# Optimization experiments

Hardware: AMD Instinct MI355X
Metric: run time of the kernel (lower is better)

Reference implementation:

```python
import jax, jax.numpy as jnp
import numpy as np

B, F, D = 16384, 40, 32

def setup_inputs() -> dict:
    key = jax.random.key(0)
    k1, k2, k3, k4 = jax.random.split(key, 4)
    g = jax.random.uniform(k1, (B, F, F), dtype=jnp.float32)
    h = jax.random.normal(k2, (B, F, D), dtype=jnp.float32)
    # Xavier-normal init for per-field [D,D] weights: std = sqrt(2/(D+D))
    std = float(np.sqrt(2.0 / (D + D)))
    W_in = jax.random.normal(k3, (F, D, D), dtype=jnp.float32) * std
    W_out = jax.random.normal(k4, (F, D, D), dtype=jnp.float32) * std
    bias_p = jnp.zeros((D,), dtype=jnp.float32)
    return {"g": g, "h": h, "W_in": W_in, "W_out": W_out, "bias_p": bias_p}

def reference(g, h, W_in, W_out, bias_p):
    # per-field transform: [F,D,D] x [B,F,D] -> [B,F,D]
    h_out = jnp.einsum('fde,bfe->bfd', W_out, h)
    # graph aggregation over fields: [B,F,F] x [B,F,D] -> [B,F,D]
    aggr = jnp.einsum('bfg,bgd->bfd', g, h_out)
    # per-field transform + bias
    a = jnp.einsum('fde,bfe->bfd', W_in, aggr) + bias_p
    return a
```

## Files before the change

### kernel.cpp

```cpp
#include <hip/hip_runtime.h>


#define B_TOT 16384
#define FF    40
#define DD    32

template<bool ADD_BIAS, bool IN_PLACE>
__global__ __launch_bounds__(256)
void field_transform(const float* __restrict__ W,
                     const float* __restrict__ src,
                     const float* __restrict__ bias,
                     float* __restrict__ dst)
{
    const int f = blockIdx.y;
    const int b = blockIdx.x * 256 + threadIdx.x;
    const float* wf = W + (size_t)f * (DD * DD);
    const float* srow = (IN_PLACE ? (const float*)dst : src)
                        + ((size_t)b * FF + f) * DD;

    float4 hr[8];
    #pragma unroll
    for (int j = 0; j < 8; ++j) hr[j] = ((const float4*)srow)[j];

    float acc[DD];
    #pragma unroll
    for (int d = 0; d < DD; ++d) {
        const float4* wrow = (const float4*)(wf + d * DD);
        float s = 0.f;
        #pragma unroll
        for (int j = 0; j < 8; ++j) {
            float4 w = wrow[j];
            s += w.x * hr[j].x + w.y * hr[j].y + w.z * hr[j].z + w.w * hr[j].w;
        }
        if (ADD_BIAS) s += bias[d];
        acc[d] = s;
    }

    float* drow = dst + ((size_t)b * FF + f) * DD;
    #pragma unroll
    for (int j = 0; j < 8; ++j)
        ((float4*)drow)[j] = make_float4(acc[4*j+0], acc[4*j+1],
                                         acc[4*j+2], acc[4*j+3]);
}

__global__ __launch_bounds__(256)
void graph_aggr(const float* __restrict__ g,
                float* __restrict__ io)
{
    __shared__ __attribute__((aligned(16))) float s_ho[4 * FF * DD];
    const int t  = threadIdx.x;
    const int b0 = blockIdx.x * 4;

    const float4* src = (const float4*)(io + (size_t)b0 * (FF * DD));
    #pragma unroll
    for (int k = 0; k < 5; ++k)
        ((float4*)s_ho)[t + k * 256] = src[t + k * 256];
    __syncthreads();

    const int w  = t >> 6;
    const int l  = t & 63;
    const int dg = l >> 3;
    const int fg = l & 7;

    const float* gb   = g + (size_t)(b0 + w) * (FF * FF);
    const float* shob = s_ho + w * (FF * DD);

    float acc[5][4];
    #pragma unroll
    for (int i = 0; i < 5; ++i)
        #pragma unroll
        for (int j = 0; j < 4; ++j) acc[i][j] = 0.f;

    for (int gc = 0; gc < 10; ++gc) {
        const int gg = gc << 2;
        float4 gv[5];
        #pragma unroll
        for (int i = 0; i < 5; ++i)
            gv[i] = *(const float4*)(gb + (fg + (i << 3)) * FF + gg);
        float4 hv0 = *(const float4*)(shob + (gg + 0) * DD + dg * 4);
        float4 hv1 = *(const float4*)(shob + (gg + 1) * DD + dg * 4);
        float4 hv2 = *(const float4*)(shob + (gg + 2) * DD + dg * 4);
        float4 hv3 = *(const float4*)(shob + (gg + 3) * DD + dg * 4);
        #pragma unroll
        for (int i = 0; i < 5; ++i) {
            acc[i][0] += gv[i].x * hv0.x + gv[i].y * hv1.x + gv[i].z * hv2.x + gv[i].w * hv3.x;
            acc[i][1] += gv[i].x * hv0.y + gv[i].y * hv1.y + gv[i].z * hv2.y + gv[i].w * hv3.y;
            acc[i][2] += gv[i].x * hv0.z + gv[i].y * hv1.z + gv[i].z * hv2.z + gv[i].w * hv3.z;
            acc[i][3] += gv[i].x * hv0.w + gv[i].y * hv1.w + gv[i].z * hv2.w + gv[i].w * hv3.w;
        }
    }

    #pragma unroll
    for (int i = 0; i < 5; ++i) {
        const int f = fg + (i << 3);
        *(float4*)(io + ((size_t)(b0 + w) * FF + f) * DD + dg * 4) =
            make_float4(acc[i][0], acc[i][1], acc[i][2], acc[i][3]);
    }
}

extern "C" void kernel_launch(void* const* d_in, const int* in_sizes, int n_in,
                              void* d_out, int out_size, void* d_ws, size_t ws_size,
                              hipStream_t stream) {
    const float* g    = (const float*)d_in[0];
    const float* h    = (const float*)d_in[1];
    const float* Win  = (const float*)d_in[2];
    const float* Wout = (const float*)d_in[3];
    const float* bias = (const float*)d_in[4];
    float* out = (float*)d_out;

    dim3 block(256);
    dim3 gridFT(B_TOT / 256, FF);
    dim3 gridAG(B_TOT / 4);

    field_transform<false, false><<<gridFT, block, 0, stream>>>(Wout, h, bias, out);
    graph_aggr<<<gridAG, block, 0, stream>>>(g, out);
    field_transform<true, true><<<gridFT, block, 0, stream>>>(Win, nullptr, bias, out);
}
```

Measured before the change: 400.3 us.

## Fuse field transforms and graph aggregation into a single kernel

Measured after the change: 526.0 us. 1.31x slower.

```diff
diff --git a/kernel.cpp b/kernel.cpp
--- a/kernel.cpp
+++ b/kernel.cpp
@@ -4,97 +4,127 @@
 #define B_TOT 16384
 #define FF    40
 #define DD    32
+#define NB    8
+#define WF    10
 
-template<bool ADD_BIAS, bool IN_PLACE>
 __global__ __launch_bounds__(256)
-void field_transform(const float* __restrict__ W,
-                     const float* __restrict__ src,
-                     const float* __restrict__ bias,
-                     float* __restrict__ dst)
+void graph_layer_fused(const float* __restrict__ g,
+                       const float* __restrict__ h,
+                       const float* __restrict__ Win,
+                       const float* __restrict__ Wout,
+                       const float* __restrict__ bias,
+                       float* __restrict__ out)
 {
-    const int f = blockIdx.y;
-    const int b = blockIdx.x * 256 + threadIdx.x;
-    const float* wf = W + (size_t)f * (DD * DD);
-    const float* srow = (IN_PLACE ? (const float*)dst : src)
-                        + ((size_t)b * FF + f) * DD;
+    __shared__ __attribute__((aligned(16))) float s_ho[NB * FF * DD];
 
-    float4 hr[8];
-    #pragma unroll
-    for (int j = 0; j < 8; ++j) hr[j] = ((const float4*)srow)[j];
+    const int t     = threadIdx.x;
+    const int w     = t >> 6;
+    const int l     = t & 63;
+    const int b0    = blockIdx.x * NB;
+    const int fbase = w * WF;
 
-    float acc[DD];
-    #pragma unroll
-    for (int d = 0; d < DD; ++d) {
-        const float4* wrow = (const float4*)(wf + d * DD);
-        float s = 0.f;
+    {
+        const int d    = l & 31;
+        const int half = l >> 5;
+        #pragma unroll 1
+        for (int fi = 0; fi < WF; ++fi) {
+            const int f = fbase + fi;
+            const float4* wrow = (const float4*)(Wout + (size_t)(f * DD + d) * DD);
+            float4 wr[8];
+            #pragma unroll
+            for (int j = 0; j < 8; ++j) wr[j] = wrow[j];
+            #pragma unroll
+            for (int bp = 0; bp < NB / 2; ++bp) {
+                const int bl = 2 * bp + half;
+                const float4* hrow =
+                    (const float4*)(h + ((size_t)(b0 + bl) * FF + f) * DD);
+                float acc = 0.f;
+                #pragma unroll
+                for (int j = 0; j < 8; ++j) {
+                    float4 hv = hrow[j];
+                    acc += wr[j].x * hv.x + wr[j].y * hv.y
+                         + wr[j].z * hv.z + wr[j].w * hv.w;
+                }
+                s_ho[(bl * FF + f) * DD + d] = acc;
+            }
+        }
+    }
+    __syncthreads();
+
+    {
+        const int bl = l >> 3;
+        const int dq = l & 7;
+        const float* grow = g + (size_t)(b0 + bl) * (FF * FF) + (size_t)fbase * FF;
+        const float* shob = s_ho + bl * (FF * DD) + dq * 4;
+
+        float4 acc[WF];
         #pragma unroll
-        for (int j = 0; j < 8; ++j) {
-            float4 w = wrow[j];
-            s += w.x * hr[j].x + w.y * hr[j].y + w.z * hr[j].z + w.w * hr[j].w;
+        for (int fi = 0; fi < WF; ++fi) acc[fi] = make_float4(0.f, 0.f, 0.f, 0.f);
+
+        float4 gv[WF];
+        #pragma unroll
+        for (int fi = 0; fi < WF; ++fi)
+            gv[fi] = *(const float4*)(grow + fi * FF);
+
+        #pragma unroll 1
+        for (int gc = 0; gc < 10; ++gc) {
+            float4 hv[4];
+            #pragma unroll
+            for (int i = 0; i < 4; ++i)
+                hv[i] = *(const float4*)(shob + (4 * gc + i) * DD);
+
+            float4 gn[WF];
+            if (gc < 9) {
+                #pragma unroll
+                for (int fi = 0; fi < WF; ++fi)
+                    gn[fi] = *(const float4*)(grow + fi * FF + 4 * gc + 4);
+            }
+
+            #pragma unroll
+            for (int fi = 0; fi < WF; ++fi) {
+                float4 gf = gv[fi];
+                acc[fi].x += gf.x*hv[0].x + gf.y*hv[1].x + gf.z*hv[2].x + gf.w*hv[3].x;
+                acc[fi].y += gf.x*hv[0].y + gf.y*hv[1].y + gf.z*hv[2].y + gf.w*hv[3].y;
+                acc[fi].z += gf.x*hv[0].z + gf.y*hv[1].z + gf.z*hv[2].z + gf.w*hv[3].z;
+                acc[fi].w += gf.x*hv[0].w + gf.y*hv[1].w + gf.z*hv[2].w + gf.w*hv[3].w;
+            }
+            #pragma unroll
+            for (int fi = 0; fi < WF; ++fi) gv[fi] = gn[fi];
         }
-        if (ADD_BIAS) s += bias[d];
-        acc[d] = s;
+
+        #pragma unroll
+        for (int fi = 0; fi < WF; ++fi)
+            *(float4*)(out + ((size_t)(b0 + bl) * FF + fbase + fi) * DD + dq * 4)
+                = acc[fi];
     }
 
-    float* drow = dst + ((size_t)b * FF + f) * DD;
-    #pragma unroll
-    for (int j = 0; j < 8; ++j)
-        ((float4*)drow)[j] = make_float4(acc[4*j+0], acc[4*j+1],
-                                         acc[4*j+2], acc[4*j+3]);
-}
+    asm volatile("s_waitcnt vmcnt(0)" ::: "memory");
 
-__global__ __launch_bounds__(256)
-void graph_aggr(const float* __restrict__ g,
-                float* __restrict__ io)
-{
-    __shared__ __attribute__((aligned(16))) float s_ho[4 * FF * DD];
-    const int t  = threadIdx.x;
-    const int b0 = blockIdx.x * 4;
-
-    const float4* src = (const float4*)(io + (size_t)b0 * (FF * DD));
-    #pragma unroll
-    for (int k = 0; k < 5; ++k)
-        ((float4*)s_ho)[t + k * 256] = src[t + k * 256];
-    __syncthreads();
-
-    const int w  = t >> 6;
-    const int l  = t & 63;
-    const int dg = l >> 3;
-    const int fg = l & 7;
-
-    const float* gb   = g + (size_t)(b0 + w) * (FF * FF);
-    const float* shob = s_ho + w * (FF * DD);
-
-    float acc[5][4];
-    #pragma unroll
-    for (int i = 0; i < 5; ++i)
-        #pragma unroll
-        for (int j = 0; j < 4; ++j) acc[i][j] = 0.f;
-
-    for (int gc = 0; gc < 10; ++gc) {
-        const int gg = gc << 2;
-        float4 gv[5];
-        #pragma unroll
-        for (int i = 0; i < 5; ++i)
-            gv[i] = *(const float4*)(gb + (fg + (i << 3)) * FF + gg);
-        float4 hv0 = *(const float4*)(shob + (gg + 0) * DD + dg * 4);
-        float4 hv1 = *(const float4*)(shob + (gg + 1) * DD + dg * 4);
-        float4 hv2 = *(const float4*)(shob + (gg + 2) * DD + dg * 4);
-        float4 hv3 = *(const float4*)(shob + (gg + 3) * DD + dg * 4);
-        #pragma unroll
-        for (int i = 0; i < 5; ++i) {
-            acc[i][0] += gv[i].x * hv0.x + gv[i].y * hv1.x + gv[i].z * hv2.x + gv[i].w * hv3.x;
-            acc[i][1] += gv[i].x * hv0.y + gv[i].y * hv1.y + gv[i].z * hv2.y + gv[i].w * hv3.y;
-            acc[i][2] += gv[i].x * hv0.z + gv[i].y * hv1.z + gv[i].z * hv2.z + gv[i].w * hv3.z;
-            acc[i][3] += gv[i].x * hv0.w + gv[i].y * hv1.w + gv[i].z * hv2.w + gv[i].w * hv3.w;
+    {
+        const int d    = l & 31;
+        const int half = l >> 5;
+        const float bv = bias[d];
+        #pragma unroll 1
+        for (int fi = 0; fi < WF; ++fi) {
+            const int f = fbase + fi;
+            const float4* wrow = (const float4*)(Win + (size_t)(f * DD + d) * DD);
+            float4 wr[8];
+            #pragma unroll
+            for (int j = 0; j < 8; ++j) wr[j] = wrow[j];
+            #pragma unroll
+            for (int bp = 0; bp < NB / 2; ++bp) {
+                const int bl = 2 * bp + half;
+                float* arow = out + ((size_t)(b0 + bl) * FF + f) * DD;
+                float acc = bv;
+                #pragma unroll
+                for (int j = 0; j < 8; ++j) {
+                    float4 av = ((const float4*)arow)[j];
+                    acc += wr[j].x * av.x + wr[j].y * av.y
+                         + wr[j].z * av.z + wr[j].w * av.w;
+                }
+                arow[d] = acc;
+            }
         }
-    }
-
-    #pragma unroll
-    for (int i = 0; i < 5; ++i) {
-        const int f = fg + (i << 3);
-        *(float4*)(io + ((size_t)(b0 + w) * FF + f) * DD + dg * 4) =
-            make_float4(acc[i][0], acc[i][1], acc[i][2], acc[i][3]);
     }
 }
 
@@ -109,10 +139,6 @@
     float* out = (float*)d_out;
 
     dim3 block(256);
-    dim3 gridFT(B_TOT / 256, FF);
-    dim3 gridAG(B_TOT / 4);
-
-    field_transform<false, false><<<gridFT, block, 0, stream>>>(Wout, h, bias, out);
-    graph_aggr<<<gridAG, block, 0, stream>>>(g, out);
-    field_transform<true, true><<<gridFT, block, 0, stream>>>(Win, nullptr, bias, out);
+    dim3 grid(B_TOT / NB);
+    graph_layer_fused<<<grid, block, 0, stream>>>(g, h, Win, Wout, bias, out);
 }
```
